# Kernel optimization log

Measured on AMD Instinct MI355X. Metric: run time of the kernel, lower is better.

The kernel has to match this reference:

```python
import jax, jax.numpy as jnp
import numpy as np

N = 100_000      # nodes
E = 1_600_000    # edges (avg degree 16)
IN = 128         # in_features
F = 64           # out_features
H = 1            # num_heads (module's broadcasting only valid for H==1)
S = 1            # num_samples
SLOPE = 0.2      # leaky relu negative slope


def setup_inputs() -> dict:
    key = jax.random.key(0)
    ks = jax.random.split(key, 6)
    feat = jax.random.normal(ks[0], (N, IN), jnp.float32)
    src = jax.random.randint(ks[1], (E,), 0, N)
    dst = jax.random.randint(ks[2], (E,), 0, N)
    noise = jax.random.normal(ks[3], (E, S, H, 1), jnp.float32)  # rsample noise
    W_fc = jax.random.normal(ks[4], (IN, H * F), jnp.float32) / np.sqrt(IN)
    W_post = jax.random.normal(ks[5], (F, 4), jnp.float32) / np.sqrt(F)
    b_post = jnp.zeros((4,), jnp.float32)
    bias = jnp.zeros((H, F), jnp.float32)
    return dict(feat=feat, W_fc=W_fc, W_post=W_post, b_post=b_post,
                bias=bias, noise=noise, src=src, dst=dst)


def reference(feat, W_fc, W_post, b_post, bias, noise, src, dst):
    # node projection: [N, IN] -> [N, H, F]
    h = (feat @ W_fc).reshape(N, H, F)
    # posterior params: [N, H, 4] -> four [N, H, 1]
    pp = h @ W_post + b_post
    loc_l, loc_r, lsl, lsr = jnp.split(pp, 4, axis=-1)
    # per-edge u_add_v gathers
    loc_e = loc_l[src] + loc_r[dst]                       # [E, H, 1]
    loc_e = jnp.where(loc_e >= 0, loc_e, SLOPE * loc_e)   # leaky relu
    scale_e = jnp.exp(lsl[src] + lsr[dst])                # [E, H, 1]
    # reparameterized sample: [E, S, H, 1]
    e = loc_e[:, None] + scale_e[:, None] * noise
    # edge softmax over incoming edges of each dst node
    emax = jax.ops.segment_max(e, dst, num_segments=N)
    e_exp = jnp.exp(e - emax[dst])
    esum = jax.ops.segment_sum(e_exp, dst, num_segments=N)
    a = e_exp / esum[dst]                                 # [E, S, H, 1]
    a = jnp.swapaxes(a, 1, -1)                            # [E, 1, H, S]
    # u_mul_e then scatter-sum to dst: [E, H, F, 1] * [E, 1, H, S]
    m = h[src][..., None] * a                             # [E, H, F, S] (H==1)
    rst = jax.ops.segment_sum(m, dst, num_segments=N)     # [N, H, F, S]
    return rst + bias[..., None]
```

## Files before the change

### kernel.cpp

```cpp
#include <hip/hip_runtime.h>
#include <math.h>

#define NSLOPE 0.2f
#define ASTRIDE 136
#define CSH 10
#define NCB 128
#define EPB 2048
#define K4T 512
#define EPT 4
#define CAPB 48
#define CBSTR 128
#define FSPLIT 16
#define SCH 1152

typedef __attribute__((ext_vector_type(8))) short bf16x8;
typedef __attribute__((ext_vector_type(4))) short bf16x4;
typedef __attribute__((ext_vector_type(4))) float f32x4;

__device__ __forceinline__ unsigned short f2bf(float x) {
    unsigned u = __float_as_uint(x);
    u += 0x7fffu + ((u >> 16) & 1u);
    return (unsigned short)(u >> 16);
}

__global__ __launch_bounds__(128) void kW(const float* __restrict__ wfc,
                                          const float* __restrict__ wpost,
                                          float4* __restrict__ wc) {
    __shared__ float wp_s[256];
    int t = threadIdx.x;
    wp_s[t] = wpost[t];
    wp_s[128 + t] = wpost[128 + t];
    __syncthreads();
    float a0 = 0.f, a1 = 0.f, a2 = 0.f, a3 = 0.f;
    for (int n = 0; n < 64; n++) {
        float w = wfc[t * 64 + n];
        a0 += w * wp_s[n * 4 + 0]; a1 += w * wp_s[n * 4 + 1];
        a2 += w * wp_s[n * 4 + 2]; a3 += w * wp_s[n * 4 + 3];
    }
    float4 o; o.x = a0; o.y = a1; o.z = a2; o.w = a3;
    wc[t] = o;
}

__global__ __launch_bounds__(256) void k1_mfma(
    const float* __restrict__ feat, const float* __restrict__ wfc,
    float4* __restrict__ h_g, int n)
{
    __shared__ unsigned short a_s[64 * ASTRIDE];
    __shared__ unsigned short b_s[64 * ASTRIDE];
    int t = threadIdx.x;
    int row0 = blockIdx.x * 64;
    for (int i = t; i < 2048; i += 256) {
        int row = i >> 5, c4 = (i & 31) * 4;
        float4 f = {0.f, 0.f, 0.f, 0.f};
        if (row0 + row < n) f = ((const float4*)(feat + (long)(row0 + row) * 128))[i & 31];
        bf16x4 b4;
        b4.x = (short)f2bf(f.x); b4.y = (short)f2bf(f.y);
        b4.z = (short)f2bf(f.z); b4.w = (short)f2bf(f.w);
        *(bf16x4*)(a_s + row * ASTRIDE + c4) = b4;
    }
    for (int i = t; i < 2048; i += 256) {
        int k = i >> 4, n0 = (i & 15) * 4;
        float4 f = ((const float4*)wfc)[i];
        b_s[(n0 + 0) * ASTRIDE + k] = f2bf(f.x);
        b_s[(n0 + 1) * ASTRIDE + k] = f2bf(f.y);
        b_s[(n0 + 2) * ASTRIDE + k] = f2bf(f.z);
        b_s[(n0 + 3) * ASTRIDE + k] = f2bf(f.w);
    }
    __syncthreads();
    int lane = t & 63, wv = t >> 6;
    int c = lane & 15, quad = lane >> 4;
    f32x4 acc[4] = {{0.f,0.f,0.f,0.f},{0.f,0.f,0.f,0.f},{0.f,0.f,0.f,0.f},{0.f,0.f,0.f,0.f}};
    int arow = wv * 16 + c;
    #pragma unroll
    for (int kb = 0; kb < 4; kb++) {
        int ko = kb * 32 + quad * 8;
        bf16x8 af = *(const bf16x8*)(a_s + arow * ASTRIDE + ko);
        #pragma unroll
        for (int tt = 0; tt < 4; tt++) {
            bf16x8 bf = *(const bf16x8*)(b_s + (tt * 16 + c) * ASTRIDE + ko);
            acc[tt] = __builtin_amdgcn_mfma_f32_16x16x32_bf16(af, bf, acc[tt], 0, 0, 0);
        }
    }
    __syncthreads();
    unsigned short* h_s = a_s;
    #pragma unroll
    for (int tt = 0; tt < 4; tt++)
        #pragma unroll
        for (int r = 0; r < 4; r++)
            h_s[(wv * 16 + quad * 4 + r) * 64 + tt * 16 + c] = f2bf(acc[tt][r]);
    __syncthreads();
    for (int i = t; i < 512; i += 256) {
        int row = i >> 3;
        if (row0 + row < n)
            h_g[(long)(row0 + row) * 8 + (i & 7)] = *(const float4*)(h_s + row * 64 + (i & 7) * 8);
    }
}

__global__ __launch_bounds__(256) void k1b_pp(
    const float* __restrict__ feat, const float4* __restrict__ wc,
    const float* __restrict__ bpost, float4* __restrict__ pp,
    int* __restrict__ fcnt, int NC, int N)
{
    int gid = blockIdx.x * 256 + threadIdx.x;
    if (gid < NC * 16) fcnt[gid] = 0;
    int wid = gid >> 6;
    int lane = threadIdx.x & 63;
    if (wid >= N) return;
    const float* fr = feat + (long)wid * 128;
    float f0 = fr[lane], f1 = fr[64 + lane];
    float4 w0 = wc[lane], w1 = wc[64 + lane];
    float p0 = f0 * w0.x + f1 * w1.x;
    float p1 = f0 * w0.y + f1 * w1.y;
    float p2 = f0 * w0.z + f1 * w1.z;
    float p3 = f0 * w0.w + f1 * w1.w;
    #pragma unroll
    for (int off = 1; off < 64; off <<= 1) {
        p0 += __shfl_xor(p0, off);
        p1 += __shfl_xor(p1, off);
        p2 += __shfl_xor(p2, off);
        p3 += __shfl_xor(p3, off);
    }
    if (lane == 0) {
        float4 bp = *((const float4*)bpost);
        float4 o;
        o.x = p0 + bp.x; o.y = p1 + bp.y; o.z = p2 + bp.z; o.w = p3 + bp.w;
        pp[wid] = o;
    }
}

__global__ __launch_bounds__(K4T) void k4a(
    const int* __restrict__ src, const int* __restrict__ dst,
    const float* __restrict__ noise, const float4* __restrict__ pp,
    int* __restrict__ counts, float2* __restrict__ cbuf, int E, int NC, int NBLK)
{
    __shared__ float    s_ev[EPB];
    __shared__ unsigned s_key[EPB];
    __shared__ unsigned char s_bin[EPB];
    __shared__ int hist[NCB], lbase[NCB], lcur[NCB];
    __shared__ int wtot;
    int t = threadIdx.x;
    int blk = blockIdx.x;
    long e0 = (long)blk * EPB;
    int d[EPT]; bool ok[EPT];
    for (int i = t; i < NCB; i += K4T) hist[i] = 0;
    __syncthreads();
    #pragma unroll
    for (int u = 0; u < EPT; u++) {
        long e = e0 + t + u * K4T;
        ok[u] = e < E;
        d[u] = ok[u] ? __builtin_nontemporal_load(dst + e) : 0;
        if (ok[u]) atomicAdd(&hist[d[u] >> CSH], 1);
    }
    __syncthreads();
    int v = (t < NCB) ? hist[t] : 0;
    int inc = v;
    #pragma unroll
    for (int off = 1; off < 64; off <<= 1) {
        int u2 = __shfl_up(inc, off);
        if ((t & 63) >= off) inc += u2;
    }
    if (t == 63) wtot = inc;
    __syncthreads();
    if (t < NCB) {
        int base = (t >= 64) ? wtot : 0;
        int lb = inc - v + base;
        lbase[t] = lb; lcur[t] = lb;
        if (t < NC) counts[blk * CBSTR + t] = v;
    }
    __syncthreads();
    #pragma unroll
    for (int u = 0; u < EPT; u++) {
        if (!ok[u]) continue;
        long e = e0 + t + u * K4T;
        int s = __builtin_nontemporal_load(src + e);
        float nz = __builtin_nontemporal_load(noise + e);
        float4 ps = pp[s], pd = pp[d[u]];
        float loc = ps.x + pd.y;
        loc = loc >= 0.f ? loc : NSLOPE * loc;
        float ev = loc + __expf(ps.z + pd.w) * nz;
        int bin = d[u] >> CSH;
        int pos = atomicAdd(&lcur[bin], 1);
        s_ev[pos] = ev;
        s_key[pos] = (unsigned)s | ((unsigned)(d[u] & 1023) << 17);
        s_bin[pos] = (unsigned char)bin;
    }
    __syncthreads();
    long rem = (long)E - e0;
    int btot = rem < EPB ? (int)rem : EPB;
    for (int i = t; i < btot; i += K4T) {
        int bin = s_bin[i];
        int slot = i - lbase[bin];
        if (slot < CAPB) {
            float2 r; r.x = s_ev[i]; r.y = __uint_as_float(s_key[i]);
            cbuf[((long)bin * NBLK + blk) * CAPB + slot] = r;
        }
    }
}

__global__ __launch_bounds__(256) void k4b(
    const int* __restrict__ counts, const float2* __restrict__ cbuf,
    int* __restrict__ fcnt, float2* __restrict__ fbuf, int NC, int NBLK, int FCAP)
{
    __shared__ float    s_ev[SCH], s_ev2[SCH];
    __shared__ unsigned s_key[SCH], s_sr2[SCH];
    __shared__ unsigned char s_sub[SCH], s_sub2[SCH];
    __shared__ int h16[16], b16[16], cur16[16], gd16[16];
    __shared__ int pfx[65];
    __shared__ int ntot;
    int t = threadIdx.x;
    int c = blockIdx.x >> 4, j = blockIdx.x & 15;
    int per = (NBLK + FSPLIT - 1) / FSPLIT;
    int blk0 = j * per;
    int nb = NBLK - blk0; if (nb > per) nb = per; if (nb < 0) nb = 0;
    if (t < 16) { h16[t] = 0; cur16[t] = 0; }
    if (t < 64) {
        int cb = 0;
        if (t < nb) {
            cb = counts[(blk0 + t) * CBSTR + c];
            if (cb > CAPB) cb = CAPB;
        }
        int inc = cb;
        #pragma unroll
        for (int off = 1; off < 64; off <<= 1) {
            int u = __shfl_up(inc, off);
            if (t >= off) inc += u;
        }
        pfx[t] = inc - cb;
        if (t == 63) { pfx[64] = inc; ntot = inc; }
    }
    __syncthreads();
    int n = ntot; if (n > SCH) n = SCH;
    for (int i = t; i < n; i += 256) {
        int lo = 0, hi = nb;
        while (hi - lo > 1) {
            int mid = (lo + hi) >> 1;
            if (pfx[mid] <= i) lo = mid; else hi = mid;
        }
        int slot = i - pfx[lo];
        float2 r = cbuf[((long)c * NBLK + blk0 + lo) * CAPB + slot];
        unsigned key = __float_as_uint(r.y);
        int sub = (key >> 23) & 15;
        s_ev[i] = r.x; s_key[i] = key; s_sub[i] = (unsigned char)sub;
        atomicAdd(&h16[sub], 1);
    }
    __syncthreads();
    if (t == 0) {
        int run = 0;
        #pragma unroll
        for (int p = 0; p < 16; p++) { b16[p] = run; run += h16[p]; }
    }
    __syncthreads();
    if (t < 16 && h16[t] > 0)
        gd16[t] = atomicAdd(&fcnt[c * 16 + t], h16[t]) - b16[t];
    __syncthreads();
    for (int i = t; i < n; i += 256) {
        int sub = s_sub[i];
        int pos = b16[sub] + atomicAdd(&cur16[sub], 1);
        unsigned key = s_key[i];
        unsigned s  = key & 0x1FFFFu;
        unsigned dl = (key >> 17) & 63u;
        s_ev2[pos] = s_ev[i];
        s_sr2[pos] = s | (dl << 26);
        s_sub2[pos] = (unsigned char)sub;
    }
    __syncthreads();
    for (int i = t; i < n; i += 256) {
        int sub = s_sub2[i];
        int gpos = gd16[sub] + i;
        if (gpos < FCAP) {
            float2 r; r.x = s_ev2[i]; r.y = __uint_as_float(s_sr2[i]);
            fbuf[(long)(c * 16 + sub) * FCAP + gpos] = r;
        }
    }
}

__global__ __launch_bounds__(256) void k56_node(
    const int* __restrict__ fcnt, const float2* __restrict__ fbuf,
    const uint4* __restrict__ h8, const float* __restrict__ bias,
    float4* __restrict__ out4, int FCAP, int N)
{
    __shared__ float    o_ev[1344 + 8];
    __shared__ unsigned o_sr[1344 + 8];
    __shared__ int c[64], ox[64], c2[64];
    int t = threadIdx.x;
    int b = blockIdx.x;
    int n0 = b << 6;
    int cnt = fcnt[b]; if (cnt > FCAP) cnt = FCAP;
    const float2* rp = fbuf + (long)b * FCAP;
    if (t < 64) { c[t] = 0; c2[t] = 0; }
    __syncthreads();
    for (int i = t; i < cnt; i += 256)
        atomicAdd(&c[__float_as_uint(rp[i].y) >> 26], 1);
    __syncthreads();
    if (t < 64) {
        int val = c[t], inc = val;
        #pragma unroll
        for (int off = 1; off < 64; off <<= 1) {
            int u = __shfl_up(inc, off);
            if (t >= off) inc += u;
        }
        ox[t] = inc - val;
    }
    __syncthreads();
    for (int i = t; i < cnt; i += 256) {
        float2 v = rp[i];
        unsigned pk = __float_as_uint(v.y);
        int dl = pk >> 26;
        int pos = ox[dl] + atomicAdd(&c2[dl], 1);
        o_ev[pos] = v.x;
        o_sr[pos] = pk & 0x03FFFFFFu;
    }
    __syncthreads();
    {
        int nn4 = t >> 2, q = t & 3;
        int cn = c[nn4];
        int i0 = ox[nn4];
        float m = -INFINITY;
        for (int i = q; i < cn; i += 4) m = fmaxf(m, o_ev[i0 + i]);
        m = fmaxf(m, __shfl_xor(m, 1));
        m = fmaxf(m, __shfl_xor(m, 2));
        float ss = 0.f;
        for (int i = q; i < cn; i += 4) {
            float w = __expf(o_ev[i0 + i] - m);
            o_ev[i0 + i] = w;
            ss += w;
        }
        ss += __shfl_xor(ss, 1);
        ss += __shfl_xor(ss, 2);
        float inv = 1.f / ss;
        for (int i = q; i < cn; i += 4) o_ev[i0 + i] *= inv;
    }
    __syncthreads();
    int lane = t & 63, wv = t >> 6;
    int ch = lane & 7, sub = lane >> 3;
    for (int r = 0; r < 16; r += 2) {
        int nnA = wv * 16 + r, nnB = nnA + 1;
        int nodeA = n0 + nnA, nodeB = n0 + nnB;
        int cA = (nodeA < N) ? c[nnA] : 0;
        int cB = (nodeB < N) ? c[nnB] : 0;
        int iA = ox[nnA], iB = ox[nnB];
        float a0[8] = {0.f,0.f,0.f,0.f,0.f,0.f,0.f,0.f};
        float a1[8] = {0.f,0.f,0.f,0.f,0.f,0.f,0.f,0.f};
        int mx = cA > cB ? cA : cB;
        for (int jb = 0; jb < mx; jb += 16) {
            bool vA0 = (jb + sub) < cA, vA1 = (jb + 8 + sub) < cA;
            bool vB0 = (jb + sub) < cB, vB1 = (jb + 8 + sub) < cB;
            int jA0 = vA0 ? iA + jb + sub     : 0;
            int jA1 = vA1 ? iA + jb + 8 + sub : 0;
            int jB0 = vB0 ? iB + jb + sub     : 0;
            int jB1 = vB1 ? iB + jb + 8 + sub : 0;
            float wA0 = vA0 ? o_ev[jA0] : 0.f; int sA0 = vA0 ? (int)o_sr[jA0] : 0;
            float wA1 = vA1 ? o_ev[jA1] : 0.f; int sA1 = vA1 ? (int)o_sr[jA1] : 0;
            float wB0 = vB0 ? o_ev[jB0] : 0.f; int sB0 = vB0 ? (int)o_sr[jB0] : 0;
            float wB1 = vB1 ? o_ev[jB1] : 0.f; int sB1 = vB1 ? (int)o_sr[jB1] : 0;
            uint4 pA0 = h8[(long)sA0 * 8 + ch];
            uint4 pA1 = h8[(long)sA1 * 8 + ch];
            uint4 pB0 = h8[(long)sB0 * 8 + ch];
            uint4 pB1 = h8[(long)sB1 * 8 + ch];
            a0[0] += wA0 * __uint_as_float(pA0.x << 16);
            a0[1] += wA0 * __uint_as_float(pA0.x & 0xffff0000u);
            a0[2] += wA0 * __uint_as_float(pA0.y << 16);
            a0[3] += wA0 * __uint_as_float(pA0.y & 0xffff0000u);
            a0[4] += wA0 * __uint_as_float(pA0.z << 16);
            a0[5] += wA0 * __uint_as_float(pA0.z & 0xffff0000u);
            a0[6] += wA0 * __uint_as_float(pA0.w << 16);
            a0[7] += wA0 * __uint_as_float(pA0.w & 0xffff0000u);
            a0[0] += wA1 * __uint_as_float(pA1.x << 16);
            a0[1] += wA1 * __uint_as_float(pA1.x & 0xffff0000u);
            a0[2] += wA1 * __uint_as_float(pA1.y << 16);
            a0[3] += wA1 * __uint_as_float(pA1.y & 0xffff0000u);
            a0[4] += wA1 * __uint_as_float(pA1.z << 16);
            a0[5] += wA1 * __uint_as_float(pA1.z & 0xffff0000u);
            a0[6] += wA1 * __uint_as_float(pA1.w << 16);
            a0[7] += wA1 * __uint_as_float(pA1.w & 0xffff0000u);
            a1[0] += wB0 * __uint_as_float(pB0.x << 16);
            a1[1] += wB0 * __uint_as_float(pB0.x & 0xffff0000u);
            a1[2] += wB0 * __uint_as_float(pB0.y << 16);
            a1[3] += wB0 * __uint_as_float(pB0.y & 0xffff0000u);
            a1[4] += wB0 * __uint_as_float(pB0.z << 16);
            a1[5] += wB0 * __uint_as_float(pB0.z & 0xffff0000u);
            a1[6] += wB0 * __uint_as_float(pB0.w << 16);
            a1[7] += wB0 * __uint_as_float(pB0.w & 0xffff0000u);
            a1[0] += wB1 * __uint_as_float(pB1.x << 16);
            a1[1] += wB1 * __uint_as_float(pB1.x & 0xffff0000u);
            a1[2] += wB1 * __uint_as_float(pB1.y << 16);
            a1[3] += wB1 * __uint_as_float(pB1.y & 0xffff0000u);
            a1[4] += wB1 * __uint_as_float(pB1.z << 16);
            a1[5] += wB1 * __uint_as_float(pB1.z & 0xffff0000u);
            a1[6] += wB1 * __uint_as_float(pB1.w << 16);
            a1[7] += wB1 * __uint_as_float(pB1.w & 0xffff0000u);
        }
        #pragma unroll
        for (int off = 8; off < 64; off <<= 1)
            #pragma unroll
            for (int i = 0; i < 8; i++) {
                a0[i] += __shfl_xor(a0[i], off);
                a1[i] += __shfl_xor(a1[i], off);
            }
        if (sub == 0) {
            const float* bl = bias + ch * 8;
            if (nodeA < N) {
                f32x4 o0, o1;
                o0[0] = a0[0] + bl[0]; o0[1] = a0[1] + bl[1]; o0[2] = a0[2] + bl[2]; o0[3] = a0[3] + bl[3];
                o1[0] = a0[4] + bl[4]; o1[1] = a0[5] + bl[5]; o1[2] = a0[6] + bl[6]; o1[3] = a0[7] + bl[7];
                __builtin_nontemporal_store(o0, (f32x4*)(out4 + (long)nodeA * 16 + ch * 2));
                __builtin_nontemporal_store(o1, (f32x4*)(out4 + (long)nodeA * 16 + ch * 2 + 1));
            }
            if (nodeB < N) {
                f32x4 o0, o1;
                o0[0] = a1[0] + bl[0]; o0[1] = a1[1] + bl[1]; o0[2] = a1[2] + bl[2]; o0[3] = a1[3] + bl[3];
                o1[0] = a1[4] + bl[4]; o1[1] = a1[5] + bl[5]; o1[2] = a1[6] + bl[6]; o1[3] = a1[7] + bl[7];
                __builtin_nontemporal_store(o0, (f32x4*)(out4 + (long)nodeB * 16 + ch * 2));
                __builtin_nontemporal_store(o1, (f32x4*)(out4 + (long)nodeB * 16 + ch * 2 + 1));
            }
        }
    }
}

extern "C" void kernel_launch(void* const* d_in, const int* in_sizes, int n_in,
                              void* d_out, int out_size, void* d_ws, size_t ws_size,
                              hipStream_t stream) {
    const float* feat  = (const float*)d_in[0];
    const float* wfc   = (const float*)d_in[1];
    const float* wpost = (const float*)d_in[2];
    const float* bpost = (const float*)d_in[3];
    const float* bias  = (const float*)d_in[4];
    const float* noise = (const float*)d_in[5];
    const int*   src   = (const int*)d_in[6];
    const int*   dst   = (const int*)d_in[7];
    int N = in_sizes[0] / 128;
    int E = in_sizes[6];
    int NC = (N + 1023) >> 10;
    int NB = (N + 63) >> 6;
    int NBLK = (E + EPB - 1) / EPB;
    int EB  = (int)((long)E * 64 / N);
    int FCAP = (EB + 8 * (int)sqrtf((float)EB) + 39) & ~7;
    if (FCAP > 1344) FCAP = 1344;

    float*  ws     = (float*)d_ws;
    float2* cbuf   = (float2*)ws;
    float2* fbuf   = (float2*)(ws + (size_t)2 * NC * NBLK * CAPB);
    float*  h      = ws + (size_t)2 * NC * NBLK * CAPB + (size_t)2 * NB * FCAP;
    float4* pp     = (float4*)(h + (size_t)32 * N);
    int*    counts = (int*)(h + (size_t)32 * N + (size_t)4 * N);
    int*    fcnt   = counts + (size_t)NBLK * CBSTR;
    float4* wc     = (float4*)(fcnt + 2048);

    hipLaunchKernelGGL(kW, dim3(1), dim3(128), 0, stream, wfc, wpost, wc);
    hipLaunchKernelGGL(k1_mfma, dim3((N + 63) / 64), dim3(256), 0, stream,
                       feat, wfc, (float4*)h, N);
    hipLaunchKernelGGL(k1b_pp, dim3((N + 3) / 4), dim3(256), 0, stream,
                       feat, wc, bpost, pp, fcnt, NC, N);
    hipLaunchKernelGGL(k4a, dim3(NBLK), dim3(K4T), 0, stream,
                       src, dst, noise, pp, counts, cbuf, E, NC, NBLK);
    hipLaunchKernelGGL(k4b, dim3(NC * FSPLIT), dim3(256), 0, stream,
                       counts, cbuf, fcnt, fbuf, NC, NBLK, FCAP);
    hipLaunchKernelGGL(k56_node, dim3(NB), dim3(256), 0, stream,
                       fcnt, fbuf, (const uint4*)h, bias, (float4*)d_out, FCAP, N);
}
```

Baseline: 245.3 us.

## Use 512-thread blocks in node kernel and cache edge records in registers

Doubles the node kernel's block size to 512 threads. Each wave now aggregates 8 nodes instead of 16, and the softmax uses 8 lanes per node. Edge records are loaded once with a nontemporal load and kept in registers for both the counting pass and the scatter pass, removing the second global read. The costs are higher register pressure and fewer resident blocks per CU.

```diff
diff --git a/kernel.cpp b/kernel.cpp
--- a/kernel.cpp
+++ b/kernel.cpp
@@ -274,7 +274,7 @@
     }
 }
 
-__global__ __launch_bounds__(256) void k56_node(
+__global__ __launch_bounds__(512) void k56_node(
     const int* __restrict__ fcnt, const float2* __restrict__ fbuf,
     const uint4* __restrict__ h8, const float* __restrict__ bias,
     float4* __restrict__ out4, int FCAP, int N)
@@ -289,8 +289,19 @@
     const float2* rp = fbuf + (long)b * FCAP;
     if (t < 64) { c[t] = 0; c2[t] = 0; }
     __syncthreads();
-    for (int i = t; i < cnt; i += 256)
-        atomicAdd(&c[__float_as_uint(rp[i].y) >> 26], 1);
+    float    revv[3];
+    unsigned rkey[3];
+    #pragma unroll
+    for (int j = 0; j < 3; j++) {
+        int i = t + j * 512;
+        if (i < cnt) {
+            unsigned long long pv = __builtin_nontemporal_load(
+                (const unsigned long long*)(rp + i));
+            revv[j] = __uint_as_float((unsigned)pv);
+            rkey[j] = (unsigned)(pv >> 32);
+            atomicAdd(&c[rkey[j] >> 26], 1);
+        }
+    }
     __syncthreads();
     if (t < 64) {
         int val = c[t], inc = val;
@@ -302,39 +313,43 @@
         ox[t] = inc - val;
     }
     __syncthreads();
-    for (int i = t; i < cnt; i += 256) {
-        float2 v = rp[i];
-        unsigned pk = __float_as_uint(v.y);
-        int dl = pk >> 26;
-        int pos = ox[dl] + atomicAdd(&c2[dl], 1);
-        o_ev[pos] = v.x;
-        o_sr[pos] = pk & 0x03FFFFFFu;
+    #pragma unroll
+    for (int j = 0; j < 3; j++) {
+        int i = t + j * 512;
+        if (i < cnt) {
+            int dl = rkey[j] >> 26;
+            int pos = ox[dl] + atomicAdd(&c2[dl], 1);
+            o_ev[pos] = revv[j];
+            o_sr[pos] = rkey[j] & 0x03FFFFFFu;
+        }
     }
     __syncthreads();
     {
-        int nn4 = t >> 2, q = t & 3;
-        int cn = c[nn4];
-        int i0 = ox[nn4];
+        int nn8 = t >> 3, q = t & 7;
+        int cn = c[nn8];
+        int i0 = ox[nn8];
         float m = -INFINITY;
-        for (int i = q; i < cn; i += 4) m = fmaxf(m, o_ev[i0 + i]);
+        for (int i = q; i < cn; i += 8) m = fmaxf(m, o_ev[i0 + i]);
         m = fmaxf(m, __shfl_xor(m, 1));
         m = fmaxf(m, __shfl_xor(m, 2));
+        m = fmaxf(m, __shfl_xor(m, 4));
         float ss = 0.f;
-        for (int i = q; i < cn; i += 4) {
+        for (int i = q; i < cn; i += 8) {
             float w = __expf(o_ev[i0 + i] - m);
             o_ev[i0 + i] = w;
             ss += w;
         }
         ss += __shfl_xor(ss, 1);
         ss += __shfl_xor(ss, 2);
+        ss += __shfl_xor(ss, 4);
         float inv = 1.f / ss;
-        for (int i = q; i < cn; i += 4) o_ev[i0 + i] *= inv;
+        for (int i = q; i < cn; i += 8) o_ev[i0 + i] *= inv;
     }
     __syncthreads();
     int lane = t & 63, wv = t >> 6;
     int ch = lane & 7, sub = lane >> 3;
-    for (int r = 0; r < 16; r += 2) {
-        int nnA = wv * 16 + r, nnB = nnA + 1;
+    for (int r = 0; r < 8; r += 2) {
+        int nnA = wv * 8 + r, nnB = nnA + 1;
         int nodeA = n0 + nnA, nodeB = n0 + nnB;
         int cA = (nodeA < N) ? c[nnA] : 0;
         int cB = (nodeB < N) ? c[nnB] : 0;
@@ -455,6 +470,6 @@
                        src, dst, noise, pp, counts, cbuf, E, NC, NBLK);
     hipLaunchKernelGGL(k4b, dim3(NC * FSPLIT), dim3(256), 0, stream,
                        counts, cbuf, fcnt, fbuf, NC, NBLK, FCAP);
-    hipLaunchKernelGGL(k56_node, dim3(NB), dim3(256), 0, stream,
+    hipLaunchKernelGGL(k56_node, dim3(NB), dim3(512), 0, stream,
                        fcnt, fbuf, (const uint4*)h, bias, (float4*)d_out, FCAP, N);
 }
```

Result: no change. 247.2 us (+0.8%).
